# Performance work log

Measured on AMD Instinct MI355X. Metric: run time of the kernel, lower is better.

The kernel has to match this reference:

```python
import jax, jax.numpy as jnp
import numpy as np
import math

M = 512          # num_bin_x
NB = 512         # num_bin_y
NUM_NODES = 2_000_000
K = 4            # max bins a node can overlap per dim (size <= 2.5 bins)
SQRT2 = math.sqrt(2.0)


def setup_inputs() -> dict:
    key = jax.random.key(0)
    k1, k2 = jax.random.split(key)
    node_pos = jax.random.uniform(k1, (NUM_NODES, 2), jnp.float32, 0.05, 0.95)
    # node sizes between 0.5 and 2.5 bins (normalized layout units)
    node_size = jax.random.uniform(k2, (NUM_NODES, 2), jnp.float32) * (2.0 / M) + (0.5 / M)
    return {
        "node_pos": node_pos,
        "node_size": node_size,
        "node_weight": jnp.ones((NUM_NODES,), jnp.float32),
        "expand_ratio": jnp.ones((NUM_NODES,), jnp.float32),
        "unit_len": jnp.array([1.0 / M, 1.0 / NB], jnp.float32),
        "init_density_map": jnp.zeros((M, NB), jnp.float32),
        "num_bin_x": M,
        "num_bin_y": NB,
    }


def pre_normalize(node_pos, node_size, node_weight, expand_ratio, unit_len, mx, ny):
    # density_map_cuda.pre_normalize: expand tiny nodes to sqrt(2)*unit_len,
    # rescale weight to preserve area, convert rects to bin coordinates.
    ux, uy = unit_len[0], unit_len[1]
    w, h = node_size[:, 0], node_size[:, 1]
    new_w = jnp.maximum(w, SQRT2 * ux)
    new_h = jnp.maximum(h, SQRT2 * uy)
    weight = node_weight * expand_ratio * (w * h) / (new_w * new_h)
    xl = jnp.clip((node_pos[:, 0] - 0.5 * new_w) / ux, 0.0, mx)
    xh = jnp.clip((node_pos[:, 0] + 0.5 * new_w) / ux, 0.0, mx)
    yl = jnp.clip((node_pos[:, 1] - 0.5 * new_h) / uy, 0.0, ny)
    yh = jnp.clip((node_pos[:, 1] + 0.5 * new_h) / uy, 0.0, ny)
    return jnp.stack([xl, xh, yl, yh, weight], axis=1)  # [N, 5]


def scatter_density(info, mx, ny):
    # density_map_cuda.forward: overlap-area scatter-add of node rects into bins.
    xl, xh, yl, yh, w = info[:, 0], info[:, 1], info[:, 2], info[:, 3], info[:, 4]
    bx0 = jnp.floor(xl).astype(jnp.int32)
    by0 = jnp.floor(yl).astype(jnp.int32)
    dm = jnp.zeros((mx, ny), jnp.float32)
    for dx in range(K):
        ix = bx0 + dx
        fx = ix.astype(jnp.float32)
        ox = jnp.clip(jnp.minimum(xh, fx + 1.0) - jnp.maximum(xl, fx), 0.0)
        ixc = jnp.clip(ix, 0, mx - 1)
        for dy in range(K):
            iy = by0 + dy
            fy = iy.astype(jnp.float32)
            oy = jnp.clip(jnp.minimum(yh, fy + 1.0) - jnp.maximum(yl, fy), 0.0)
            iyc = jnp.clip(iy, 0, ny - 1)
            dm = dm.at[ixc, iyc].add(w * ox * oy)
    return dm


def make_transforms(n):
    k = jnp.arange(n, dtype=jnp.float32)[:, None]
    m = jnp.arange(n, dtype=jnp.float32)[None, :]
    ang = jnp.pi * k * (2.0 * m + 1.0) / (2.0 * n)
    C = jnp.cos(ang)  # [freq, space]
    S = jnp.sin(ang)
    w = jnp.where(jnp.arange(n) == 0, 1.0, 2.0).astype(jnp.float32)
    return C, S, w


def spectral_solve(dm, unit_len, mx, ny):
    # fft_scale construction from __init__
    wj = (jnp.arange(mx, dtype=jnp.float32) * (2.0 * jnp.pi / mx))[:, None]
    wk = (jnp.arange(ny, dtype=jnp.float32) * (2.0 * jnp.pi / ny))[None, :]
    wk = wk * (unit_len[0] / unit_len[1])  # scale_w_k=True
    wsq = wj ** 2 + wk ** 2
    wsq = wsq.at[0, 0].set(1.0)
    pscale = (1.0 / wsq).at[0, 0].set(0.0)
    fx_scale = wj * pscale * 0.5
    fy_scale = wk * pscale * 0.5

    Cx, Sx, wx = make_transforms(mx)
    Cy, Sy, wy = make_transforms(ny)
    # dct2: coeff[u,v] = (1/(M*N)) * sum_{m,n} dm[m,n] cos(pi u(2m+1)/2M) cos(pi v(2n+1)/2N)
    coeff = (Cx @ dm @ Cy.T) / (mx * ny)
    ICx = (wx[:, None] * Cx)  # weighted inverse cosine basis [freq, space]
    ICy = (wy[:, None] * Cy)
    ISx = (wx[:, None] * Sx)
    ISy = (wy[:, None] * Sy)
    potential = ICx.T @ (coeff * pscale) @ ICy          # idct2
    force_x = ISx.T @ (coeff * fx_scale) @ ICy          # idxst_idct
    force_y = ICx.T @ (coeff * fy_scale) @ ISy          # idct_idxst
    return potential, force_x, force_y


def reference(node_pos, node_size, node_weight, expand_ratio, unit_len,
              init_density_map, num_bin_x, num_bin_y):
    info = pre_normalize(node_pos, node_size, node_weight, expand_ratio,
                         unit_len, num_bin_x, num_bin_y)
    density_map = init_density_map + scatter_density(info, num_bin_x, num_bin_y)
    potential, _, _ = spectral_solve(density_map, unit_len, num_bin_x, num_bin_y)
    energy = jnp.sum(potential * density_map)
    return energy
```

## Files before the change

kernel.cpp:

```cpp
#include <hip/hip_runtime.h>
#include <math.h>

#define MX 512
#define NY 512
#define TWO_PI 6.283185307179586f

#define TSHIFT 6
#define NT 64
#define LDIM 68
#define SLAB (LDIM * LDIM)
#define SLAB4 (SLAB / 4)
#define NPB 2048
#define KPT 8
#define CAP 40960
#define SPTMAX 32
#define RPARTS 19
#define QSCALE 26214.0f
#define QINV (1.0f / 26214.0f)

typedef __attribute__((ext_vector_type(8))) short short8;
typedef __attribute__((ext_vector_type(4))) float float4_t;
typedef __attribute__((ext_vector_type(4))) unsigned short ushort4_t;

__device__ __forceinline__ unsigned short f2bf(float x) {
    union { float f; unsigned u; } v; v.f = x;
    unsigned r = v.u + 0x7fffu + ((v.u >> 16) & 1u);
    return (unsigned short)(r >> 16);
}
__device__ __forceinline__ float bf2f(unsigned short h) {
    union { float f; unsigned u; } v; v.u = ((unsigned)h) << 16;
    return v.f;
}

__device__ __forceinline__ void node_bounds(float2 p, float2 s, float ux, float uy,
                                            float& xl, float& xh, float& yl, float& yh,
                                            float& nw, float& nh) {
    const float SQ2 = 1.41421356237309515f;
    nw = fmaxf(s.x, SQ2 * ux);
    nh = fmaxf(s.y, SQ2 * uy);
    xl = fminf(fmaxf((p.x - 0.5f * nw) / ux, 0.0f), (float)MX);
    xh = fminf(fmaxf((p.x + 0.5f * nw) / ux, 0.0f), (float)MX);
    yl = fminf(fmaxf((p.y - 0.5f * nh) / uy, 0.0f), (float)NY);
    yh = fminf(fmaxf((p.y + 0.5f * nh) / uy, 0.0f), (float)NY);
}

__global__ void gen_cos_kernel(unsigned short* __restrict__ Ch,
                               unsigned short* __restrict__ Cl,
                               unsigned int* __restrict__ base,
                               unsigned int* __restrict__ cursor,
                               float* __restrict__ out, int cap_mode) {
    int idx = blockIdx.x * blockDim.x + threadIdx.x;
    if (idx == 0) *out = 0.0f;
    if (cap_mode && idx <= NT) {
        base[idx] = (unsigned int)idx * CAP;
        if (idx < NT) cursor[idx] = (unsigned int)idx * CAP;
    }
    int a = idx >> 9;
    int j = idx & 511;
    float x = cospif((float)(a * (2 * j + 1)) * (1.0f / 1024.0f));
    unsigned short hi = f2bf(x);
    Ch[idx] = hi;
    Cl[idx] = f2bf(x - bf2f(hi));
}

__global__ __launch_bounds__(256)
void count_kernel(const float2* __restrict__ pos, const float2* __restrict__ size,
                  const float* __restrict__ unit_len,
                  unsigned int* __restrict__ cnt, int n) {
    __shared__ unsigned int h[NT];
    if (threadIdx.x < NT) h[threadIdx.x] = 0;
    __syncthreads();
    float ux = unit_len[0], uy = unit_len[1];
    int start = blockIdx.x * NPB;
    int end = min(start + NPB, n);
#pragma unroll
    for (int k = 0; k < KPT; k++) {
        int i = start + k * 256 + (int)threadIdx.x;
        if (i < end) {
            float xl, xh, yl, yh, nw, nh;
            node_bounds(pos[i], size[i], ux, uy, xl, xh, yl, yh, nw, nh);
            int bx0 = min((int)floorf(xl), MX - 1);
            int by0 = min((int)floorf(yl), NY - 1);
            atomicAdd(&h[((bx0 >> TSHIFT) << 3) | (by0 >> TSHIFT)], 1u);
        }
    }
    __syncthreads();
    if (threadIdx.x < NT) {
        unsigned int c = h[threadIdx.x];
        if (c) atomicAdd(&cnt[threadIdx.x], c);
    }
}

__global__ void scan_kernel(const unsigned int* __restrict__ cnt,
                            unsigned int* __restrict__ base,
                            unsigned int* __restrict__ cursor) {
    if (threadIdx.x == 0 && blockIdx.x == 0) {
        unsigned int ex = 0;
        for (int t = 0; t < NT; t++) {
            base[t] = ex;
            cursor[t] = ex;
            ex += cnt[t];
        }
        base[NT] = ex;
    }
}

__global__ __launch_bounds__(256)
void place_kernel(const float2* __restrict__ pos, const float2* __restrict__ size,
                  const float* __restrict__ nwt, const float* __restrict__ er,
                  const float* __restrict__ unit_len,
                  const unsigned int* __restrict__ base,
                  unsigned int* __restrict__ cursor,
                  float4* __restrict__ pb, int n) {
    __shared__ unsigned int h[NT];
    __shared__ unsigned int lb[NT + 1];
    __shared__ unsigned int bb[NT];
    __shared__ float4 buf[NPB];
    __shared__ unsigned char til[NPB];
    if (threadIdx.x < NT) h[threadIdx.x] = 0;
    __syncthreads();
    float ux = unit_len[0], uy = unit_len[1];
    int start = blockIdx.x * NPB;
    int end = min(start + NPB, n);

    float cxl[KPT], cyl[KPT], cw[KPT];
    unsigned int cq[KPT], pk[KPT];
#pragma unroll
    for (int k = 0; k < KPT; k++) {
        int i = start + k * 256 + (int)threadIdx.x;
        if (i < end) {
            float2 p = pos[i], s = size[i];
            float xl, xh, yl, yh, nw, nh;
            node_bounds(p, s, ux, uy, xl, xh, yl, yh, nw, nh);
            cxl[k] = xl; cyl[k] = yl;
            cw[k] = nwt[i] * er[i] * (s.x * s.y) / (nw * nh);
            unsigned qx = (unsigned)((xh - xl) * QSCALE + 0.5f);
            unsigned qy = (unsigned)((yh - yl) * QSCALE + 0.5f);
            if (qx > 65535u) qx = 65535u;
            if (qy > 65535u) qy = 65535u;
            cq[k] = qx | (qy << 16);
            int bx0 = min((int)floorf(xl), MX - 1);
            int by0 = min((int)floorf(yl), NY - 1);
            unsigned int t = ((bx0 >> TSHIFT) << 3) | (by0 >> TSHIFT);
            pk[k] = (t << 11) | atomicAdd(&h[t], 1u);
        }
    }
    __syncthreads();
    if (threadIdx.x == 0) {
        unsigned int ex = 0;
        for (int t = 0; t < NT; t++) { lb[t] = ex; ex += h[t]; }
        lb[NT] = ex;
    }
    if (threadIdx.x < NT) {
        unsigned int c = h[threadIdx.x];
        bb[threadIdx.x] = c ? atomicAdd(&cursor[threadIdx.x], c) : 0u;
    }
    __syncthreads();
#pragma unroll
    for (int k = 0; k < KPT; k++) {
        int i = start + k * 256 + (int)threadIdx.x;
        if (i < end) {
            unsigned int t = pk[k] >> 11;
            unsigned int slot = lb[t] + (pk[k] & 2047u);
            buf[slot] = make_float4(cxl[k], cyl[k], cw[k], __uint_as_float(cq[k]));
            til[slot] = (unsigned char)t;
        }
    }
    __syncthreads();
    unsigned int total = lb[NT];
    for (unsigned int j = threadIdx.x; j < total; j += 256) {
        unsigned int t = til[j];
        unsigned int dst = bb[t] + (j - lb[t]);
        if (dst < base[t + 1]) pb[dst] = buf[j];
    }
}

__device__ __forceinline__ void accum_one(float4 v, float* acc, int tbx, int tby) {
    float xl = v.x, yl = v.y, w = v.z;
    unsigned q = __float_as_uint(v.w);
    float xh = xl + (float)(q & 0xffffu) * QINV;
    float yh = yl + (float)(q >> 16) * QINV;
    int bx0 = min((int)floorf(xl), MX - 1);
    int by0 = min((int)floorf(yl), NY - 1);
    float oxs[4], oys[4];
    int rb[4], lys[4];
#pragma unroll
    for (int d = 0; d < 4; d++) {
        int ix = bx0 + d;
        float fx = (float)ix;
        oxs[d] = fmaxf(fminf(xh, fx + 1.0f) - fmaxf(xl, fx), 0.0f);
        rb[d] = (min(ix, MX - 1) - tbx) * LDIM;
        int iy = by0 + d;
        float fy = (float)iy;
        oys[d] = fmaxf(fminf(yh, fy + 1.0f) - fmaxf(yl, fy), 0.0f);
        lys[d] = min(iy, NY - 1) - tby;
    }
#pragma unroll
    for (int dx = 0; dx < 4; dx++) {
        if (oxs[dx] == 0.0f) continue;
        float wox = w * oxs[dx];
#pragma unroll
        for (int dy = 0; dy < 4; dy++) {
            float vv = wox * oys[dy];
            if (vv != 0.0f) atomicAdd(&acc[rb[dx] + lys[dy]], vv);
        }
    }
}

__global__ __launch_bounds__(256)
void accum_kernel(const float4* __restrict__ pb,
                  const unsigned int* __restrict__ base,
                  const unsigned int* __restrict__ cursor,
                  float* __restrict__ slab, int spt) {
    __shared__ float acc[SLAB];
    int t = blockIdx.x / spt;
    int s = blockIdx.x - t * spt;
    int tbx = (t >> 3) << TSHIFT;
    int tby = (t & 7) << TSHIFT;
    for (int e = threadIdx.x; e < SLAB4; e += 256)
        ((float4*)acc)[e] = make_float4(0.f, 0.f, 0.f, 0.f);
    __syncthreads();

    unsigned int b0 = base[t];
    unsigned int c = min(cursor[t] - b0, base[t + 1] - b0);
    unsigned int chunk = (c + spt - 1) / spt;
    unsigned int ks = s * chunk;
    unsigned int ke = min(c, ks + chunk);

    unsigned int k = ks + threadIdx.x;
    float4 cur = make_float4(0.f, 0.f, 0.f, 0.f);
    bool have = (k < ke);
    if (have) cur = pb[b0 + k];
    while (have) {
        unsigned int k2 = k + 256;
        bool have2 = (k2 < ke);
        float4 nxt = make_float4(0.f, 0.f, 0.f, 0.f);
        if (have2) nxt = pb[b0 + k2];
        accum_one(cur, acc, tbx, tby);
        cur = nxt; k = k2; have = have2;
    }
    __syncthreads();

    float4* dst = (float4*)(slab + (size_t)blockIdx.x * SLAB);
    for (int e = threadIdx.x; e < SLAB4; e += 256)
        dst[e] = ((float4*)acc)[e];
}

__global__ __launch_bounds__(256)
void reduce_slabs_kernel(const float* __restrict__ slab,
                         float* __restrict__ tacc, int spt) {
    int t = blockIdx.x / RPARTS;
    int part = blockIdx.x - t * RPARTS;
    int e = part * 256 + (int)threadIdx.x;
    if (e < SLAB) {
        const float* s0 = slab + (size_t)t * spt * SLAB + e;
        float sum = 0.0f;
        for (int s = 0; s < spt; s++) sum += s0[(size_t)s * SLAB];
        tacc[(size_t)t * SLAB + e] = sum;
    }
}

__global__ __launch_bounds__(256)
void combine_kernel(const float* __restrict__ tacc,
                    const float* __restrict__ init_dm,
                    unsigned short* __restrict__ dmh,
                    unsigned short* __restrict__ dml) {
    int v = blockIdx.x * blockDim.x + threadIdx.x;
    int gx = v >> 7;
    int g4 = v & 127;
    int gy = g4 << 2;
    int rx = gx & 63, ry = gy & 63;
    int tx0 = gx >> TSHIFT, ty0 = gy >> TSHIFT;

    float4 sum = ((const float4*)init_dm)[v];
#pragma unroll
    for (int ax = 0; ax < 2; ax++) {
        int tx = tx0 - ax;
        if (tx < 0 || (ax == 1 && rx > 3)) continue;
        int lx = rx + (ax << TSHIFT);
#pragma unroll
        for (int ay = 0; ay < 2; ay++) {
            int ty = ty0 - ay;
            if (ty < 0 || (ay == 1 && ry > 0)) continue;
            int ly = ry + (ay << TSHIFT);
            float4 sv = *(const float4*)(tacc
                + (size_t)((tx << 3) | ty) * SLAB + lx * LDIM + ly);
            sum.x += sv.x; sum.y += sv.y; sum.z += sv.z; sum.w += sv.w;
        }
    }
    ushort4_t hi, lo;
    float sv[4] = {sum.x, sum.y, sum.z, sum.w};
#pragma unroll
    for (int r = 0; r < 4; r++) {
        unsigned short h = f2bf(sv[r]);
        hi[r] = h;
        lo[r] = f2bf(sv[r] - bf2f(h));
    }
    int idx = (gx << 9) | gy;
    *(ushort4_t*)(dmh + idx) = hi;
    *(ushort4_t*)(dml + idx) = lo;
}

__global__ __launch_bounds__(256)
void scatter_kernel(const float2* __restrict__ pos, const float2* __restrict__ size,
                    const float* __restrict__ nwt, const float* __restrict__ er,
                    const float* __restrict__ unit_len,
                    float* __restrict__ dm, int n) {
    int i = blockIdx.x * blockDim.x + threadIdx.x;
    if (i >= n) return;
    float ux = unit_len[0], uy = unit_len[1];
    float2 p = pos[i], s = size[i];
    float xl, xh, yl, yh, nw, nh;
    node_bounds(p, s, ux, uy, xl, xh, yl, yh, nw, nh);
    float w = nwt[i] * er[i] * (s.x * s.y) / (nw * nh);
    int bx0 = (int)floorf(xl);
    int by0 = (int)floorf(yl);
#pragma unroll
    for (int dx = 0; dx < 4; dx++) {
        int ix = bx0 + dx;
        float fx = (float)ix;
        float ox = fmaxf(fminf(xh, fx + 1.0f) - fmaxf(xl, fx), 0.0f);
        if (ox == 0.0f) continue;
        int rowoff = min(max(ix, 0), MX - 1) * NY;
        float wox = w * ox;
#pragma unroll
        for (int dy = 0; dy < 4; dy++) {
            int iy = by0 + dy;
            float fy = (float)iy;
            float oy = fmaxf(fminf(yh, fy + 1.0f) - fmaxf(yl, fy), 0.0f);
            float vv = wox * oy;
            if (vv != 0.0f) atomicAdd(&dm[rowoff + min(max(iy, 0), NY - 1)], vv);
        }
    }
}

__global__ void cvt_dm_kernel(const float* __restrict__ dm,
                              unsigned short* __restrict__ dmh,
                              unsigned short* __restrict__ dml) {
    int idx = blockIdx.x * blockDim.x + threadIdx.x;
    float x = dm[idx];
    unsigned short hi = f2bf(x);
    dmh[idx] = hi;
    dml[idx] = f2bf(x - bf2f(hi));
}

__global__ __launch_bounds__(256)
void dct1_mfma_kernel(const unsigned short* __restrict__ dmh,
                      const unsigned short* __restrict__ dml,
                      const unsigned short* __restrict__ Ch,
                      const unsigned short* __restrict__ Cl,
                      unsigned short* __restrict__ UhT,
                      unsigned short* __restrict__ UlT) {
    int lane = threadIdx.x & 63;
    int wv = threadIdx.x >> 6;
    int tile = blockIdx.x * 4 + wv;
    int jt = (tile >> 5) * 16;
    int bt = (tile & 31) * 16;
    int m = lane & 15, q = lane >> 4;
    float4_t acc = {0.f, 0.f, 0.f, 0.f};
    const unsigned short* ah_row = dmh + (jt + m) * 512;
    const unsigned short* al_row = dml + (jt + m) * 512;
    const unsigned short* bh_row = Ch + (bt + m) * 512;
    const unsigned short* bl_row = Cl + (bt + m) * 512;
#pragma unroll 4
    for (int k0 = 0; k0 < 512; k0 += 32) {
        int off = k0 + q * 8;
        short8 ah = *(const short8*)(ah_row + off);
        short8 al = *(const short8*)(al_row + off);
        short8 bh = *(const short8*)(bh_row + off);
        short8 bl = *(const short8*)(bl_row + off);
        acc = __builtin_amdgcn_mfma_f32_16x16x32_bf16(ah, bh, acc, 0, 0, 0);
        acc = __builtin_amdgcn_mfma_f32_16x16x32_bf16(ah, bl, acc, 0, 0, 0);
        acc = __builtin_amdgcn_mfma_f32_16x16x32_bf16(al, bh, acc, 0, 0, 0);
    }
#pragma unroll
    for (int r = 0; r < 4; r++) {
        float v = acc[r];
        unsigned short hi = f2bf(v);
        int addr = (bt + m) * 512 + jt + q * 4 + r;
        UhT[addr] = hi;
        UlT[addr] = f2bf(v - bf2f(hi));
    }
}

__global__ __launch_bounds__(256)
void dct2_mfma_kernel(const unsigned short* __restrict__ Ch,
                      const unsigned short* __restrict__ Cl,
                      const unsigned short* __restrict__ UhT,
                      const unsigned short* __restrict__ UlT,
                      const float* __restrict__ unit_len,
                      float* __restrict__ out) {
    __shared__ float red[4];
    int lane = threadIdx.x & 63;
    int wv = threadIdx.x >> 6;
    int tile = blockIdx.x * 4 + wv;
    int at = (tile >> 5) * 16;
    int bt = (tile & 31) * 16;
    int m = lane & 15, q = lane >> 4;
    float4_t acc = {0.f, 0.f, 0.f, 0.f};
    const unsigned short* ah_row = Ch + (at + m) * 512;
    const unsigned short* al_row = Cl + (at + m) * 512;
    const unsigned short* bh_row = UhT + (bt + m) * 512;
    const unsigned short* bl_row = UlT + (bt + m) * 512;
#pragma unroll 4
    for (int k0 = 0; k0 < 512; k0 += 32) {
        int off = k0 + q * 8;
        short8 ah = *(const short8*)(ah_row + off);
        short8 al = *(const short8*)(al_row + off);
        short8 bh = *(const short8*)(bh_row + off);
        short8 bl = *(const short8*)(bl_row + off);
        acc = __builtin_amdgcn_mfma_f32_16x16x32_bf16(ah, bh, acc, 0, 0, 0);
        acc = __builtin_amdgcn_mfma_f32_16x16x32_bf16(ah, bl, acc, 0, 0, 0);
        acc = __builtin_amdgcn_mfma_f32_16x16x32_bf16(al, bh, acc, 0, 0, 0);
    }
    float ratio = unit_len[0] / unit_len[1];
    int b = bt + m;
    float wkb = (float)b * (TWO_PI / (float)NY) * ratio;
    float wyb = (b == 0) ? 1.0f : 2.0f;
    float e = 0.0f;
#pragma unroll
    for (int r = 0; r < 4; r++) {
        int a = at + q * 4 + r;
        float wja = (float)a * (TWO_PI / (float)MX);
        float wsq = wja * wja + wkb * wkb;
        float ps = (a == 0 && b == 0) ? 0.0f : (1.0f / wsq);
        float wxa = (a == 0) ? 1.0f : 2.0f;
        e += wxa * wyb * ps * acc[r] * acc[r];
    }
#pragma unroll
    for (int off = 32; off > 0; off >>= 1) e += __shfl_down(e, off, 64);
    if (lane == 0) red[wv] = e;
    __syncthreads();
    if (threadIdx.x == 0) {
        float t = red[0] + red[1] + red[2] + red[3];
        atomicAdd(out, t * (1.0f / ((float)MX * (float)NY)));
    }
}

extern "C" void kernel_launch(void* const* d_in, const int* in_sizes, int n_in,
                              void* d_out, int out_size, void* d_ws, size_t ws_size,
                              hipStream_t stream) {
    const float2* node_pos  = (const float2*)d_in[0];
    const float2* node_size = (const float2*)d_in[1];
    const float*  node_wt   = (const float*)d_in[2];
    const float*  exp_ratio = (const float*)d_in[3];
    const float*  unit_len  = (const float*)d_in[4];
    const float*  init_dm   = (const float*)d_in[5];
    float* out = (float*)d_out;
    int n = in_sizes[2];

    char* wsb = (char*)d_ws;
    size_t off = 0;
    auto alloc = [&](size_t bytes) { void* p = wsb + off; off = (off + bytes + 255) & ~(size_t)255; return p; };
    unsigned short* Ch   = (unsigned short*)alloc((size_t)MX * NY * 2);
    unsigned short* Cl   = (unsigned short*)alloc((size_t)MX * NY * 2);
    unsigned short* dmh  = (unsigned short*)alloc((size_t)MX * NY * 2);
    unsigned short* dml  = (unsigned short*)alloc((size_t)MX * NY * 2);
    unsigned short* UhT  = (unsigned short*)alloc((size_t)MX * NY * 2);
    unsigned short* UlT  = (unsigned short*)alloc((size_t)MX * NY * 2);
    float*          dm     = (float*)alloc((size_t)MX * NY * sizeof(float));
    unsigned int*   cnt    = (unsigned int*)alloc(NT * sizeof(unsigned int));
    unsigned int*   tbase  = (unsigned int*)alloc((NT + 1) * sizeof(unsigned int));
    unsigned int*   cursor = (unsigned int*)alloc(NT * sizeof(unsigned int));
    float*          tacc   = (float*)alloc((size_t)NT * SLAB * sizeof(float));
    size_t off_common = off;
    size_t per_spt = (size_t)NT * SLAB * sizeof(float);

    float4* pbF = (float4*)alloc((size_t)NT * CAP * sizeof(float4));
    int sptF = 0;
    float* slbF = nullptr;
    if (off <= ws_size) {
        sptF = (int)((ws_size - off) / per_spt);
        if (sptF > SPTMAX) sptF = SPTMAX;
        if (sptF >= 4) slbF = (float*)alloc((size_t)NT * sptF * SLAB * sizeof(float));
    }
    bool tierFast = (slbF != nullptr);

    off = off_common;
    float4* pbE = (float4*)alloc((size_t)n * sizeof(float4));
    int sptE = 0;
    float* slbE = nullptr;
    if (off <= ws_size) {
        sptE = (int)((ws_size - off) / per_spt);
        if (sptE > SPTMAX) sptE = SPTMAX;
        if (sptE >= 1) slbE = (float*)alloc((size_t)NT * sptE * SLAB * sizeof(float));
    }
    bool tierExact = (slbE != nullptr);

    gen_cos_kernel<<<(MX * NY) / 256, 256, 0, stream>>>(Ch, Cl, tbase, cursor,
                                                        out, tierFast ? 1 : 0);

    if (tierFast || tierExact) {
        float4* pb  = tierFast ? pbF : pbE;
        float*  slb = tierFast ? slbF : slbE;
        int     spt = tierFast ? sptF : sptE;
        int nblk = (n + NPB - 1) / NPB;
        if (!tierFast) {
            hipMemsetAsync(cnt, 0, NT * sizeof(unsigned int), stream);
            count_kernel<<<nblk, 256, 0, stream>>>(node_pos, node_size, unit_len, cnt, n);
            scan_kernel<<<1, 64, 0, stream>>>(cnt, tbase, cursor);
        }
        place_kernel<<<nblk, 256, 0, stream>>>(
            node_pos, node_size, node_wt, exp_ratio, unit_len, tbase, cursor, pb, n);
        accum_kernel<<<NT * spt, 256, 0, stream>>>(pb, tbase, cursor, slb, spt);
        reduce_slabs_kernel<<<NT * RPARTS, 256, 0, stream>>>(slb, tacc, spt);
        combine_kernel<<<256, 256, 0, stream>>>(tacc, init_dm, dmh, dml);
    } else {
        hipMemcpyAsync(dm, init_dm, (size_t)MX * NY * sizeof(float),
                       hipMemcpyDeviceToDevice, stream);
        scatter_kernel<<<(n + 255) / 256, 256, 0, stream>>>(
            node_pos, node_size, node_wt, exp_ratio, unit_len, dm, n);
        cvt_dm_kernel<<<(MX * NY) / 256, 256, 0, stream>>>(dm, dmh, dml);
    }

    dct1_mfma_kernel<<<256, 256, 0, stream>>>(dmh, dml, Ch, Cl, UhT, UlT);
    dct2_mfma_kernel<<<256, 256, 0, stream>>>(Ch, Cl, UhT, UlT, unit_len, out);
}
```

Baseline: 240.5 us.

## Fuse slab reduction, combine, and both DCT stages into one cooperative kernel

Replaces the separate reduce_slabs, combine, dct1 and dct2 launches with a single cooperative kernel of 256 blocks that uses grid-wide syncs between phases. Cosine table generation also moves into this kernel, and a tiny init kernel handles the per-tile base and cursor setup. The aim is to remove several kernel launch gaps and inter-kernel bubbles at the tail of the pipeline. In exchange, the slab reduction now runs on only 65536 threads instead of the previous larger grid, and grid.sync carries its own overhead.

```diff
diff --git a/kernel.cpp b/kernel.cpp
--- a/kernel.cpp
+++ b/kernel.cpp
@@ -1,5 +1,8 @@
 #include <hip/hip_runtime.h>
+#include <hip/hip_cooperative_groups.h>
 #include <math.h>
+
+namespace cg = cooperative_groups;
 
 #define MX 512
 #define NY 512
@@ -14,7 +17,6 @@
 #define KPT 8
 #define CAP 40960
 #define SPTMAX 32
-#define RPARTS 19
 #define QSCALE 26214.0f
 #define QINV (1.0f / 26214.0f)
 
@@ -44,23 +46,15 @@
     yh = fminf(fmaxf((p.y + 0.5f * nh) / uy, 0.0f), (float)NY);
 }
 
-__global__ void gen_cos_kernel(unsigned short* __restrict__ Ch,
-                               unsigned short* __restrict__ Cl,
-                               unsigned int* __restrict__ base,
-                               unsigned int* __restrict__ cursor,
-                               float* __restrict__ out, int cap_mode) {
-    int idx = blockIdx.x * blockDim.x + threadIdx.x;
-    if (idx == 0) *out = 0.0f;
-    if (cap_mode && idx <= NT) {
-        base[idx] = (unsigned int)idx * CAP;
-        if (idx < NT) cursor[idx] = (unsigned int)idx * CAP;
-    }
-    int a = idx >> 9;
-    int j = idx & 511;
-    float x = cospif((float)(a * (2 * j + 1)) * (1.0f / 1024.0f));
-    unsigned short hi = f2bf(x);
-    Ch[idx] = hi;
-    Cl[idx] = f2bf(x - bf2f(hi));
+__global__ void init_kernel(unsigned int* __restrict__ base,
+                            unsigned int* __restrict__ cursor,
+                            float* __restrict__ out, int cap_mode) {
+    int t = threadIdx.x;
+    if (t == 0) *out = 0.0f;
+    if (cap_mode && t <= NT) {
+        base[t] = (unsigned int)t * CAP;
+        if (t < NT) cursor[t] = (unsigned int)t * CAP;
+    }
 }
 
 __global__ __launch_bounds__(256)
@@ -247,58 +241,162 @@
 }
 
 __global__ __launch_bounds__(256)
-void reduce_slabs_kernel(const float* __restrict__ slab,
-                         float* __restrict__ tacc, int spt) {
-    int t = blockIdx.x / RPARTS;
-    int part = blockIdx.x - t * RPARTS;
-    int e = part * 256 + (int)threadIdx.x;
-    if (e < SLAB) {
-        const float* s0 = slab + (size_t)t * spt * SLAB + e;
+void fused_tail_kernel(const float* __restrict__ slab, float* __restrict__ tacc,
+                       const float* __restrict__ init_dm,
+                       unsigned short* __restrict__ dmh, unsigned short* __restrict__ dml,
+                       unsigned short* __restrict__ Ch, unsigned short* __restrict__ Cl,
+                       unsigned short* __restrict__ UhT, unsigned short* __restrict__ UlT,
+                       const float* __restrict__ unit_len, float* __restrict__ out,
+                       int spt) {
+    cg::grid_group grid = cg::this_grid();
+    __shared__ float red[4];
+    int tid = blockIdx.x * 256 + (int)threadIdx.x;
+
+#pragma unroll
+    for (int r = 0; r < 4; r++) {
+        int idx = tid + r * 65536;
+        int a = idx >> 9, j = idx & 511;
+        float x = cospif((float)(a * (2 * j + 1)) * (1.0f / 1024.0f));
+        unsigned short hi = f2bf(x);
+        Ch[idx] = hi;
+        Cl[idx] = f2bf(x - bf2f(hi));
+    }
+    for (int e = tid; e < NT * SLAB; e += 65536) {
+        int t = e / SLAB;
+        int off = e - t * SLAB;
+        const float* s0 = slab + (size_t)t * spt * SLAB + off;
         float sum = 0.0f;
         for (int s = 0; s < spt; s++) sum += s0[(size_t)s * SLAB];
-        tacc[(size_t)t * SLAB + e] = sum;
-    }
-}
-
-__global__ __launch_bounds__(256)
-void combine_kernel(const float* __restrict__ tacc,
-                    const float* __restrict__ init_dm,
-                    unsigned short* __restrict__ dmh,
-                    unsigned short* __restrict__ dml) {
-    int v = blockIdx.x * blockDim.x + threadIdx.x;
-    int gx = v >> 7;
-    int g4 = v & 127;
-    int gy = g4 << 2;
-    int rx = gx & 63, ry = gy & 63;
-    int tx0 = gx >> TSHIFT, ty0 = gy >> TSHIFT;
-
-    float4 sum = ((const float4*)init_dm)[v];
-#pragma unroll
-    for (int ax = 0; ax < 2; ax++) {
-        int tx = tx0 - ax;
-        if (tx < 0 || (ax == 1 && rx > 3)) continue;
-        int lx = rx + (ax << TSHIFT);
-#pragma unroll
-        for (int ay = 0; ay < 2; ay++) {
-            int ty = ty0 - ay;
-            if (ty < 0 || (ay == 1 && ry > 0)) continue;
-            int ly = ry + (ay << TSHIFT);
-            float4 sv = *(const float4*)(tacc
-                + (size_t)((tx << 3) | ty) * SLAB + lx * LDIM + ly);
-            sum.x += sv.x; sum.y += sv.y; sum.z += sv.z; sum.w += sv.w;
-        }
-    }
-    ushort4_t hi, lo;
-    float sv[4] = {sum.x, sum.y, sum.z, sum.w};
-#pragma unroll
-    for (int r = 0; r < 4; r++) {
-        unsigned short h = f2bf(sv[r]);
-        hi[r] = h;
-        lo[r] = f2bf(sv[r] - bf2f(h));
-    }
-    int idx = (gx << 9) | gy;
-    *(ushort4_t*)(dmh + idx) = hi;
-    *(ushort4_t*)(dml + idx) = lo;
+        tacc[e] = sum;
+    }
+    grid.sync();
+
+    {
+        int gx = tid >> 7;
+        int gy = (tid & 127) << 2;
+        int rx = gx & 63, ry = gy & 63;
+        int tx0 = gx >> TSHIFT, ty0 = gy >> TSHIFT;
+        float4 sum = ((const float4*)init_dm)[tid];
+#pragma unroll
+        for (int ax = 0; ax < 2; ax++) {
+            int tx = tx0 - ax;
+            if (tx < 0 || (ax == 1 && rx > 3)) continue;
+            int lx = rx + (ax << TSHIFT);
+#pragma unroll
+            for (int ay = 0; ay < 2; ay++) {
+                int ty = ty0 - ay;
+                if (ty < 0 || (ay == 1 && ry > 0)) continue;
+                int ly = ry + (ay << TSHIFT);
+                float4 sv = *(const float4*)(tacc
+                    + (size_t)((tx << 3) | ty) * SLAB + lx * LDIM + ly);
+                sum.x += sv.x; sum.y += sv.y; sum.z += sv.z; sum.w += sv.w;
+            }
+        }
+        ushort4_t hi, lo;
+        float sv[4] = {sum.x, sum.y, sum.z, sum.w};
+#pragma unroll
+        for (int r = 0; r < 4; r++) {
+            unsigned short h = f2bf(sv[r]);
+            hi[r] = h;
+            lo[r] = f2bf(sv[r] - bf2f(h));
+        }
+        int idx = (gx << 9) | gy;
+        *(ushort4_t*)(dmh + idx) = hi;
+        *(ushort4_t*)(dml + idx) = lo;
+    }
+    grid.sync();
+
+    int lane = threadIdx.x & 63;
+    int wv = threadIdx.x >> 6;
+    int m = lane & 15, q = lane >> 4;
+
+    {
+        int tile = blockIdx.x * 4 + wv;
+        int jt = (tile >> 5) * 16;
+        int bt = (tile & 31) * 16;
+        float4_t acc = {0.f, 0.f, 0.f, 0.f};
+        const unsigned short* ah_row = dmh + (jt + m) * 512;
+        const unsigned short* al_row = dml + (jt + m) * 512;
+        const unsigned short* bh_row = Ch + (bt + m) * 512;
+        const unsigned short* bl_row = Cl + (bt + m) * 512;
+#pragma unroll 4
+        for (int k0 = 0; k0 < 512; k0 += 32) {
+            int off = k0 + q * 8;
+            short8 ah = *(const short8*)(ah_row + off);
+            short8 al = *(const short8*)(al_row + off);
+            short8 bh = *(const short8*)(bh_row + off);
+            short8 bl = *(const short8*)(bl_row + off);
+            acc = __builtin_amdgcn_mfma_f32_16x16x32_bf16(ah, bh, acc, 0, 0, 0);
+            acc = __builtin_amdgcn_mfma_f32_16x16x32_bf16(ah, bl, acc, 0, 0, 0);
+            acc = __builtin_amdgcn_mfma_f32_16x16x32_bf16(al, bh, acc, 0, 0, 0);
+        }
+#pragma unroll
+        for (int r = 0; r < 4; r++) {
+            float v = acc[r];
+            unsigned short hi = f2bf(v);
+            int addr = (bt + m) * 512 + jt + q * 4 + r;
+            UhT[addr] = hi;
+            UlT[addr] = f2bf(v - bf2f(hi));
+        }
+    }
+    grid.sync();
+
+    {
+        int tile = blockIdx.x * 4 + wv;
+        int at = (tile >> 5) * 16;
+        int bt = (tile & 31) * 16;
+        float4_t acc = {0.f, 0.f, 0.f, 0.f};
+        const unsigned short* ah_row = Ch + (at + m) * 512;
+        const unsigned short* al_row = Cl + (at + m) * 512;
+        const unsigned short* bh_row = UhT + (bt + m) * 512;
+        const unsigned short* bl_row = UlT + (bt + m) * 512;
+#pragma unroll 4
+        for (int k0 = 0; k0 < 512; k0 += 32) {
+            int off = k0 + q * 8;
+            short8 ah = *(const short8*)(ah_row + off);
+            short8 al = *(const short8*)(al_row + off);
+            short8 bh = *(const short8*)(bh_row + off);
+            short8 bl = *(const short8*)(bl_row + off);
+            acc = __builtin_amdgcn_mfma_f32_16x16x32_bf16(ah, bh, acc, 0, 0, 0);
+            acc = __builtin_amdgcn_mfma_f32_16x16x32_bf16(ah, bl, acc, 0, 0, 0);
+            acc = __builtin_amdgcn_mfma_f32_16x16x32_bf16(al, bh, acc, 0, 0, 0);
+        }
+        float ratio = unit_len[0] / unit_len[1];
+        int b = bt + m;
+        float wkb = (float)b * (TWO_PI / (float)NY) * ratio;
+        float wyb = (b == 0) ? 1.0f : 2.0f;
+        float e = 0.0f;
+#pragma unroll
+        for (int r = 0; r < 4; r++) {
+            int a = at + q * 4 + r;
+            float wja = (float)a * (TWO_PI / (float)MX);
+            float wsq = wja * wja + wkb * wkb;
+            float ps = (a == 0 && b == 0) ? 0.0f : (1.0f / wsq);
+            float wxa = (a == 0) ? 1.0f : 2.0f;
+            e += wxa * wyb * ps * acc[r] * acc[r];
+        }
+#pragma unroll
+        for (int off = 32; off > 0; off >>= 1) e += __shfl_down(e, off, 64);
+        if (lane == 0) red[wv] = e;
+        __syncthreads();
+        if (threadIdx.x == 0) {
+            float t = red[0] + red[1] + red[2] + red[3];
+            atomicAdd(out, t * (1.0f / ((float)MX * (float)NY)));
+        }
+    }
+}
+
+__global__ void gen_cos_kernel(unsigned short* __restrict__ Ch,
+                               unsigned short* __restrict__ Cl,
+                               float* __restrict__ out) {
+    int idx = blockIdx.x * blockDim.x + threadIdx.x;
+    if (idx == 0) *out = 0.0f;
+    int a = idx >> 9;
+    int j = idx & 511;
+    float x = cospif((float)(a * (2 * j + 1)) * (1.0f / 1024.0f));
+    unsigned short hi = f2bf(x);
+    Ch[idx] = hi;
+    Cl[idx] = f2bf(x - bf2f(hi));
 }
 
 __global__ __launch_bounds__(256)
@@ -487,14 +585,12 @@
     }
     bool tierExact = (slbE != nullptr);
 
-    gen_cos_kernel<<<(MX * NY) / 256, 256, 0, stream>>>(Ch, Cl, tbase, cursor,
-                                                        out, tierFast ? 1 : 0);
-
     if (tierFast || tierExact) {
         float4* pb  = tierFast ? pbF : pbE;
         float*  slb = tierFast ? slbF : slbE;
         int     spt = tierFast ? sptF : sptE;
         int nblk = (n + NPB - 1) / NPB;
+        init_kernel<<<1, 128, 0, stream>>>(tbase, cursor, out, tierFast ? 1 : 0);
         if (!tierFast) {
             hipMemsetAsync(cnt, 0, NT * sizeof(unsigned int), stream);
             count_kernel<<<nblk, 256, 0, stream>>>(node_pos, node_size, unit_len, cnt, n);
@@ -503,16 +599,22 @@
         place_kernel<<<nblk, 256, 0, stream>>>(
             node_pos, node_size, node_wt, exp_ratio, unit_len, tbase, cursor, pb, n);
         accum_kernel<<<NT * spt, 256, 0, stream>>>(pb, tbase, cursor, slb, spt);
-        reduce_slabs_kernel<<<NT * RPARTS, 256, 0, stream>>>(slb, tacc, spt);
-        combine_kernel<<<256, 256, 0, stream>>>(tacc, init_dm, dmh, dml);
+        void* kargs[] = {
+            (void*)&slb, (void*)&tacc, (void*)&init_dm,
+            (void*)&dmh, (void*)&dml, (void*)&Ch, (void*)&Cl,
+            (void*)&UhT, (void*)&UlT, (void*)&unit_len, (void*)&out,
+            (void*)&spt
+        };
+        hipLaunchCooperativeKernel((void*)fused_tail_kernel, dim3(256), dim3(256),
+                                   kargs, 0, stream);
     } else {
+        gen_cos_kernel<<<(MX * NY) / 256, 256, 0, stream>>>(Ch, Cl, out);
         hipMemcpyAsync(dm, init_dm, (size_t)MX * NY * sizeof(float),
                        hipMemcpyDeviceToDevice, stream);
         scatter_kernel<<<(n + 255) / 256, 256, 0, stream>>>(
             node_pos, node_size, node_wt, exp_ratio, unit_len, dm, n);
         cvt_dm_kernel<<<(MX * NY) / 256, 256, 0, stream>>>(dm, dmh, dml);
-    }
-
-    dct1_mfma_kernel<<<256, 256, 0, stream>>>(dmh, dml, Ch, Cl, UhT, UlT);
-    dct2_mfma_kernel<<<256, 256, 0, stream>>>(Ch, Cl, UhT, UlT, unit_len, out);
-}
+        dct1_mfma_kernel<<<256, 256, 0, stream>>>(dmh, dml, Ch, Cl, UhT, UlT);
+        dct2_mfma_kernel<<<256, 256, 0, stream>>>(Ch, Cl, UhT, UlT, unit_len, out);
+    }
+}
```

Result: slower. 373.2 us (+55.2%).

## Replace shared-memory atomic scatter with per-bin gather over counting-sorted node batches

Applied to the files above, without the earlier changes.

The per-tile accumulation kernel no longer scatters with LDS atomics. It counting-sorts each batch of nodes by their home bin in shared memory, and each thread then gathers contributions for its own output bins from the up to 4x4 neighbouring home bins, keeping the sums in registers. This removes atomic contention on hot bins, but adds a block-wide prefix scan per batch, many barriers, and a divergent, data-dependent gather loop. Register pressure from the 19-entry accumulator array may also reduce occupancy. The scatter and convert kernels are only moved within the file.

```diff
diff --git a/kernel.cpp b/kernel.cpp
--- a/kernel.cpp
+++ b/kernel.cpp
@@ -15,6 +15,7 @@
 #define CAP 40960
 #define SPTMAX 32
 #define RPARTS 19
+#define BATCH 1280
 #define QSCALE 26214.0f
 #define QINV (1.0f / 26214.0f)
 
@@ -175,75 +176,114 @@
     }
 }
 
-__device__ __forceinline__ void accum_one(float4 v, float* acc, int tbx, int tby) {
-    float xl = v.x, yl = v.y, w = v.z;
-    unsigned q = __float_as_uint(v.w);
-    float xh = xl + (float)(q & 0xffffu) * QINV;
-    float yh = yl + (float)(q >> 16) * QINV;
-    int bx0 = min((int)floorf(xl), MX - 1);
-    int by0 = min((int)floorf(yl), NY - 1);
-    float oxs[4], oys[4];
-    int rb[4], lys[4];
-#pragma unroll
-    for (int d = 0; d < 4; d++) {
-        int ix = bx0 + d;
-        float fx = (float)ix;
-        oxs[d] = fmaxf(fminf(xh, fx + 1.0f) - fmaxf(xl, fx), 0.0f);
-        rb[d] = (min(ix, MX - 1) - tbx) * LDIM;
-        int iy = by0 + d;
-        float fy = (float)iy;
-        oys[d] = fmaxf(fminf(yh, fy + 1.0f) - fmaxf(yl, fy), 0.0f);
-        lys[d] = min(iy, NY - 1) - tby;
-    }
-#pragma unroll
-    for (int dx = 0; dx < 4; dx++) {
-        if (oxs[dx] == 0.0f) continue;
-        float wox = w * oxs[dx];
-#pragma unroll
-        for (int dy = 0; dy < 4; dy++) {
-            float vv = wox * oys[dy];
-            if (vv != 0.0f) atomicAdd(&acc[rb[dx] + lys[dy]], vv);
-        }
-    }
-}
-
-__global__ __launch_bounds__(256)
-void accum_kernel(const float4* __restrict__ pb,
-                  const unsigned int* __restrict__ base,
-                  const unsigned int* __restrict__ cursor,
-                  float* __restrict__ slab, int spt) {
-    __shared__ float acc[SLAB];
+__global__ __launch_bounds__(256)
+void accum_gather_kernel(const float4* __restrict__ pb,
+                         const unsigned int* __restrict__ base,
+                         const unsigned int* __restrict__ cursor,
+                         float* __restrict__ slab, int spt) {
+    __shared__ unsigned int cur[4096];
+    __shared__ float4 snode[BATCH];
+    __shared__ unsigned int partial[256];
     int t = blockIdx.x / spt;
     int s = blockIdx.x - t * spt;
     int tbx = (t >> 3) << TSHIFT;
     int tby = (t & 7) << TSHIFT;
-    for (int e = threadIdx.x; e < SLAB4; e += 256)
-        ((float4*)acc)[e] = make_float4(0.f, 0.f, 0.f, 0.f);
-    __syncthreads();
-
-    unsigned int b0 = base[t];
-    unsigned int c = min(cursor[t] - b0, base[t + 1] - b0);
+
+    unsigned int b0g = base[t];
+    unsigned int c = min(cursor[t] - b0g, base[t + 1] - b0g);
     unsigned int chunk = (c + spt - 1) / spt;
     unsigned int ks = s * chunk;
     unsigned int ke = min(c, ks + chunk);
 
-    unsigned int k = ks + threadIdx.x;
-    float4 cur = make_float4(0.f, 0.f, 0.f, 0.f);
-    bool have = (k < ke);
-    if (have) cur = pb[b0 + k];
-    while (have) {
-        unsigned int k2 = k + 256;
-        bool have2 = (k2 < ke);
-        float4 nxt = make_float4(0.f, 0.f, 0.f, 0.f);
-        if (have2) nxt = pb[b0 + k2];
-        accum_one(cur, acc, tbx, tby);
-        cur = nxt; k = k2; have = have2;
-    }
-    __syncthreads();
-
-    float4* dst = (float4*)(slab + (size_t)blockIdx.x * SLAB);
-    for (int e = threadIdx.x; e < SLAB4; e += 256)
-        dst[e] = ((float4*)acc)[e];
+    float acc[19];
+#pragma unroll
+    for (int j = 0; j < 19; j++) acc[j] = 0.0f;
+
+    for (unsigned int bs = ks; bs < ke; bs += BATCH) {
+        unsigned int bn = min((unsigned int)BATCH, ke - bs);
+        for (int e = threadIdx.x; e < 4096; e += 256) cur[e] = 0;
+        __syncthreads();
+        float4 nd[5];
+        int hm[5];
+#pragma unroll
+        for (int k = 0; k < 5; k++) {
+            unsigned int idx = (unsigned)k * 256u + threadIdx.x;
+            hm[k] = -1;
+            if (idx < bn) {
+                float4 v = pb[b0g + bs + idx];
+                nd[k] = v;
+                int hlx = min((int)floorf(v.x), MX - 1) - tbx;
+                int hly = min((int)floorf(v.y), NY - 1) - tby;
+                hm[k] = (hlx << 6) | hly;
+                atomicAdd(&cur[hm[k]], 1u);
+            }
+        }
+        __syncthreads();
+        unsigned int ssum = 0;
+#pragma unroll
+        for (int e = 0; e < 16; e++) ssum += cur[threadIdx.x * 16 + e];
+        partial[threadIdx.x] = ssum;
+        __syncthreads();
+        for (int o = 1; o < 256; o <<= 1) {
+            unsigned int v = (threadIdx.x >= (unsigned)o) ? partial[threadIdx.x - o] : 0u;
+            __syncthreads();
+            partial[threadIdx.x] += v;
+            __syncthreads();
+        }
+        unsigned int run = (threadIdx.x == 0) ? 0u : partial[threadIdx.x - 1];
+#pragma unroll
+        for (int e = 0; e < 16; e++) {
+            unsigned int i2 = threadIdx.x * 16 + e;
+            unsigned int tmp = cur[i2];
+            cur[i2] = run;
+            run += tmp;
+        }
+        __syncthreads();
+        #pragma unroll
+        for (int k = 0; k < 5; k++) {
+            if (hm[k] >= 0) {
+                unsigned int off = atomicAdd(&cur[hm[k]], 1u);
+                snode[off] = nd[k];
+            }
+        }
+        __syncthreads();
+#pragma unroll
+        for (int j = 0; j < 19; j++) {
+            int l = (int)threadIdx.x + (j << 8);
+            if (l < SLAB) {
+                int lx = l / LDIM;
+                int ly = l - lx * LDIM;
+                int hxa = max(lx - 3, 0), hxb = min(lx, 63);
+                int hya = max(ly - 3, 0), hyb = min(ly, 63);
+                if (hxa <= hxb && hya <= hyb) {
+                    float X = (float)(tbx + lx), Y = (float)(tby + ly);
+                    float a = acc[j];
+                    for (int hx = hxa; hx <= hxb; hx++) {
+                        int bb0 = (hx << 6) + hya;
+                        int bb1 = (hx << 6) + hyb;
+                        unsigned int st = bb0 ? cur[bb0 - 1] : 0u;
+                        unsigned int en = cur[bb1];
+                        for (unsigned int k = st; k < en; k++) {
+                            float4 v = snode[k];
+                            unsigned int q = __float_as_uint(v.w);
+                            float xh = v.x + (float)(q & 0xffffu) * QINV;
+                            float yh = v.y + (float)(q >> 16) * QINV;
+                            float ox = fmaxf(fminf(xh, X + 1.0f) - fmaxf(v.x, X), 0.0f);
+                            float oy = fmaxf(fminf(yh, Y + 1.0f) - fmaxf(v.y, Y), 0.0f);
+                            a += v.z * ox * oy;
+                        }
+                    }
+                    acc[j] = a;
+                }
+            }
+        }
+        __syncthreads();
+    }
+#pragma unroll
+    for (int j = 0; j < 19; j++) {
+        int l = (int)threadIdx.x + (j << 8);
+        if (l < SLAB) slab[(size_t)blockIdx.x * SLAB + l] = acc[j];
+    }
 }
 
 __global__ __launch_bounds__(256)
@@ -299,49 +339,6 @@
     int idx = (gx << 9) | gy;
     *(ushort4_t*)(dmh + idx) = hi;
     *(ushort4_t*)(dml + idx) = lo;
-}
-
-__global__ __launch_bounds__(256)
-void scatter_kernel(const float2* __restrict__ pos, const float2* __restrict__ size,
-                    const float* __restrict__ nwt, const float* __restrict__ er,
-                    const float* __restrict__ unit_len,
-                    float* __restrict__ dm, int n) {
-    int i = blockIdx.x * blockDim.x + threadIdx.x;
-    if (i >= n) return;
-    float ux = unit_len[0], uy = unit_len[1];
-    float2 p = pos[i], s = size[i];
-    float xl, xh, yl, yh, nw, nh;
-    node_bounds(p, s, ux, uy, xl, xh, yl, yh, nw, nh);
-    float w = nwt[i] * er[i] * (s.x * s.y) / (nw * nh);
-    int bx0 = (int)floorf(xl);
-    int by0 = (int)floorf(yl);
-#pragma unroll
-    for (int dx = 0; dx < 4; dx++) {
-        int ix = bx0 + dx;
-        float fx = (float)ix;
-        float ox = fmaxf(fminf(xh, fx + 1.0f) - fmaxf(xl, fx), 0.0f);
-        if (ox == 0.0f) continue;
-        int rowoff = min(max(ix, 0), MX - 1) * NY;
-        float wox = w * ox;
-#pragma unroll
-        for (int dy = 0; dy < 4; dy++) {
-            int iy = by0 + dy;
-            float fy = (float)iy;
-            float oy = fmaxf(fminf(yh, fy + 1.0f) - fmaxf(yl, fy), 0.0f);
-            float vv = wox * oy;
-            if (vv != 0.0f) atomicAdd(&dm[rowoff + min(max(iy, 0), NY - 1)], vv);
-        }
-    }
-}
-
-__global__ void cvt_dm_kernel(const float* __restrict__ dm,
-                              unsigned short* __restrict__ dmh,
-                              unsigned short* __restrict__ dml) {
-    int idx = blockIdx.x * blockDim.x + threadIdx.x;
-    float x = dm[idx];
-    unsigned short hi = f2bf(x);
-    dmh[idx] = hi;
-    dml[idx] = f2bf(x - bf2f(hi));
 }
 
 __global__ __launch_bounds__(256)
@@ -437,6 +434,49 @@
     }
 }
 
+__global__ __launch_bounds__(256)
+void scatter_kernel(const float2* __restrict__ pos, const float2* __restrict__ size,
+                    const float* __restrict__ nwt, const float* __restrict__ er,
+                    const float* __restrict__ unit_len,
+                    float* __restrict__ dm, int n) {
+    int i = blockIdx.x * blockDim.x + threadIdx.x;
+    if (i >= n) return;
+    float ux = unit_len[0], uy = unit_len[1];
+    float2 p = pos[i], s = size[i];
+    float xl, xh, yl, yh, nw, nh;
+    node_bounds(p, s, ux, uy, xl, xh, yl, yh, nw, nh);
+    float w = nwt[i] * er[i] * (s.x * s.y) / (nw * nh);
+    int bx0 = (int)floorf(xl);
+    int by0 = (int)floorf(yl);
+#pragma unroll
+    for (int dx = 0; dx < 4; dx++) {
+        int ix = bx0 + dx;
+        float fx = (float)ix;
+        float ox = fmaxf(fminf(xh, fx + 1.0f) - fmaxf(xl, fx), 0.0f);
+        if (ox == 0.0f) continue;
+        int rowoff = min(max(ix, 0), MX - 1) * NY;
+        float wox = w * ox;
+#pragma unroll
+        for (int dy = 0; dy < 4; dy++) {
+            int iy = by0 + dy;
+            float fy = (float)iy;
+            float oy = fmaxf(fminf(yh, fy + 1.0f) - fmaxf(yl, fy), 0.0f);
+            float vv = wox * oy;
+            if (vv != 0.0f) atomicAdd(&dm[rowoff + min(max(iy, 0), NY - 1)], vv);
+        }
+    }
+}
+
+__global__ void cvt_dm_kernel(const float* __restrict__ dm,
+                              unsigned short* __restrict__ dmh,
+                              unsigned short* __restrict__ dml) {
+    int idx = blockIdx.x * blockDim.x + threadIdx.x;
+    float x = dm[idx];
+    unsigned short hi = f2bf(x);
+    dmh[idx] = hi;
+    dml[idx] = f2bf(x - bf2f(hi));
+}
+
 extern "C" void kernel_launch(void* const* d_in, const int* in_sizes, int n_in,
                               void* d_out, int out_size, void* d_ws, size_t ws_size,
                               hipStream_t stream) {
@@ -502,7 +542,7 @@
         }
         place_kernel<<<nblk, 256, 0, stream>>>(
             node_pos, node_size, node_wt, exp_ratio, unit_len, tbase, cursor, pb, n);
-        accum_kernel<<<NT * spt, 256, 0, stream>>>(pb, tbase, cursor, slb, spt);
+        accum_gather_kernel<<<NT * spt, 256, 0, stream>>>(pb, tbase, cursor, slb, spt);
         reduce_slabs_kernel<<<NT * RPARTS, 256, 0, stream>>>(slb, tacc, spt);
         combine_kernel<<<256, 256, 0, stream>>>(tacc, init_dm, dmh, dml);
     } else {
```

Result: slower. 372.4 us (+54.8%).
